# Kernel tuning notes

Measured on AMD Instinct MI355X. Metric: run time of the kernel, lower is better.

The kernel has to match this reference:

```python
import jax, jax.numpy as jnp
import numpy as np

N_HEADS = 16
ROPE_BASE = 10000.0


def apply_rope(x):
    # x: [B, H, T, D]; rotate interleaved pairs along last dim, positions along T
    B, H, T, D = x.shape
    half = D // 2
    inv_freq = 1.0 / (ROPE_BASE ** (jnp.arange(0, half, dtype=jnp.float32) * 2.0 / D))
    angles = jnp.arange(T, dtype=jnp.float32)[:, None] * inv_freq[None, :]  # [T, half]
    cos = jnp.cos(angles).astype(x.dtype)  # [T, half]
    sin = jnp.sin(angles).astype(x.dtype)
    xp = x.reshape(B, H, T, half, 2)
    x1, x2 = xp[..., 0], xp[..., 1]
    out = jnp.stack([x1 * cos - x2 * sin, x1 * sin + x2 * cos], axis=-1)
    return out.reshape(B, H, T, D)


def setup_inputs() -> dict:
    key = jax.random.key(0)
    k1, k2, k3 = jax.random.split(key, 3)
    C = 1024
    x = jax.random.normal(k1, (2, 2048, C), dtype=jnp.float32)
    w_qkv = jax.random.normal(k2, (C, 3 * C), dtype=jnp.float32) * (1.0 / np.sqrt(C))
    w_out = jax.random.normal(k3, (C, C), dtype=jnp.float32) * (1.0 / np.sqrt(C))
    return {"x": x, "w_qkv": w_qkv, "w_out": w_out}


def reference(x, w_qkv, w_out):
    B, T, C = x.shape
    H = N_HEADS
    D = C // H
    qkv = (x @ w_qkv).reshape(B, T, 3, H, D)
    q, k, v = qkv[:, :, 0], qkv[:, :, 1], qkv[:, :, 2]  # [B, T, H, D]
    q = jnp.transpose(q, (0, 2, 1, 3))  # [B, H, T, D]
    k = jnp.transpose(k, (0, 2, 1, 3))
    v = jnp.transpose(v, (0, 2, 1, 3))
    q = apply_rope(q)
    k = apply_rope(k)
    scale = 1.0 / np.sqrt(D)
    scores = jnp.einsum('bhqd,bhkd->bhqk', q, k) * scale
    causal = jnp.tril(jnp.ones((T, T), dtype=bool))
    scores = jnp.where(causal, scores, jnp.finfo(scores.dtype).min)
    attn = jax.nn.softmax(scores, axis=-1)
    out = jnp.einsum('bhqk,bhkd->bhqd', attn, v)  # [B, H, T, D]
    out = jnp.transpose(out, (0, 2, 1, 3)).reshape(B, T, C)
    return out @ w_out
```

## Files before the change

### kernel.cpp

```cpp
#include <hip/hip_runtime.h>
#include <hip/hip_bf16.h>

typedef __attribute__((ext_vector_type(8))) short v8s;
typedef __attribute__((ext_vector_type(4))) float v4f;
typedef __attribute__((ext_vector_type(16))) float v16f;

typedef const __attribute__((address_space(1))) void* gas_ptr;
typedef __attribute__((address_space(3))) void* las_ptr;

#define MFMA16(a, b, c) __builtin_amdgcn_mfma_f32_16x16x32_bf16((a), (b), (c), 0, 0, 0)
#define MFMA32(a, b, c) __builtin_amdgcn_mfma_f32_32x32x16_bf16((a), (b), (c), 0, 0, 0)

__device__ __forceinline__ void gload_lds16(const void* g, void* l) {
  __builtin_amdgcn_global_load_lds((gas_ptr)g, (las_ptr)l, 16, 0, 0);
}

__device__ __forceinline__ unsigned short f2bf(float f) {
  unsigned int u = __float_as_uint(f);
  u += 0x7FFFu + ((u >> 16) & 1u);
  return (unsigned short)(u >> 16);
}
__device__ __forceinline__ float bf2f(unsigned short h) {
  return __uint_as_float(((unsigned int)h) << 16);
}

__device__ __forceinline__ unsigned cvt_pk_bf16(float lo, float hi) {
  unsigned r;
  asm("v_cvt_pk_bf16_f32 %0, %1, %2" : "=v"(r) : "v"(lo), "v"(hi));
  return r;
}

__global__ __launch_bounds__(256) void k_convert(const float* __restrict__ in,
                                                 unsigned short* __restrict__ out, int n4) {
  int i = blockIdx.x * 256 + threadIdx.x;
  if (i >= n4) return;
  float4 v = ((const float4*)in)[i];
  ushort4 o;
  o.x = f2bf(v.x); o.y = f2bf(v.y); o.z = f2bf(v.z); o.w = f2bf(v.w);
  ((ushort4*)out)[i] = o;
}

__global__ __launch_bounds__(256) void k_transpose_convert(const float* __restrict__ in,
                                                           unsigned short* __restrict__ out,
                                                           int R, int C) {
  __shared__ __attribute__((aligned(16))) unsigned short tb[64 * 72];
  const int r0 = blockIdx.y * 64, c0 = blockIdx.x * 64;
  const int tid = threadIdx.x;
#pragma unroll
  for (int j = 0; j < 4; ++j) {
    int slot = tid + 256 * j;
    int row = slot >> 4, q4 = (slot & 15) * 4;
    float4 v = *(const float4*)&in[(size_t)(r0 + row) * C + c0 + q4];
    ushort4 o;
    o.x = f2bf(v.x); o.y = f2bf(v.y); o.z = f2bf(v.z); o.w = f2bf(v.w);
    *(ushort4*)&tb[row * 72 + q4] = o;
  }
  __syncthreads();
#pragma unroll
  for (int j = 0; j < 4; ++j) {
    int slot = tid + 256 * j;
    int crow = slot >> 4, t4 = (slot & 15) * 4;
    ushort4 o;
    o.x = tb[(t4 + 0) * 72 + crow];
    o.y = tb[(t4 + 1) * 72 + crow];
    o.z = tb[(t4 + 2) * 72 + crow];
    o.w = tb[(t4 + 3) * 72 + crow];
    *(ushort4*)&out[(size_t)(c0 + crow) * R + r0 + t4] = o;
  }
}

template <bool F32OUT, int BN, int WAVES_M, int WAVES_N>
__global__ __launch_bounds__(256) void k_gemm(const unsigned short* __restrict__ A,
                                              const unsigned short* __restrict__ Bt,
                                              void* __restrict__ Cout,
                                              int M, int N, int K) {
  constexpr int WM = 128 / (WAVES_M * 16);
  constexpr int WN = BN / (WAVES_N * 16);
  __shared__ __attribute__((aligned(16))) unsigned short As[128 * 32];
  __shared__ __attribute__((aligned(16))) unsigned short Bs[BN * 32];
  const int tid = threadIdx.x;
  const int w = tid >> 6, l = tid & 63, g = l >> 4, c = l & 15;
  const int wr = w / WAVES_N, wc = w % WAVES_N;

  const int nwg = gridDim.x * gridDim.y;
  const int orig = blockIdx.y * gridDim.x + blockIdx.x;
  const int wgid = (orig & 7) * (nwg >> 3) + (orig >> 3);
  const int mt = (wgid / gridDim.x) * 128;
  const int nt = (wgid % gridDim.x) * BN;

  const int rowc = l >> 2, kslot = (l & 3) * 8;

  v4f acc[WM][WN];
#pragma unroll
  for (int m = 0; m < WM; ++m)
#pragma unroll
    for (int n = 0; n < WN; ++n) acc[m][n] = (v4f){0.f, 0.f, 0.f, 0.f};

  constexpr int NCHUNK = 8 + BN / 16;
  for (int kt = 0; kt < K; kt += 32) {
    __syncthreads();
#pragma unroll
    for (int ch = 0; ch < NCHUNK; ch += 4) {
      int cc = ch + w;
      if (cc < 8)
        gload_lds16(&A[(size_t)(mt + cc * 16 + rowc) * K + kt + kslot], &As[cc * 512]);
      else
        gload_lds16(&Bt[(size_t)(nt + (cc - 8) * 16 + rowc) * K + kt + kslot],
                    &Bs[(cc - 8) * 512]);
    }
    __syncthreads();
    v8s af[WM], bfr[WN];
#pragma unroll
    for (int m = 0; m < WM; ++m)
      af[m] = *(const v8s*)&As[(wr * (WM * 16) + m * 16 + c) * 32 + g * 8];
#pragma unroll
    for (int n = 0; n < WN; ++n)
      bfr[n] = *(const v8s*)&Bs[(wc * (WN * 16) + n * 16 + c) * 32 + g * 8];
#pragma unroll
    for (int m = 0; m < WM; ++m)
#pragma unroll
      for (int n = 0; n < WN; ++n)
        acc[m][n] = MFMA16(af[m], bfr[n], acc[m][n]);
  }

#pragma unroll
  for (int m = 0; m < WM; ++m)
#pragma unroll
    for (int n = 0; n < WN; ++n)
#pragma unroll
      for (int r = 0; r < 4; ++r) {
        int row = mt + wr * (WM * 16) + m * 16 + g * 4 + r;
        int col = nt + wc * (WN * 16) + n * 16 + c;
        if (F32OUT)
          ((float*)Cout)[(size_t)row * N + col] = acc[m][n][r];
        else
          ((unsigned short*)Cout)[(size_t)row * N + col] = f2bf(acc[m][n][r]);
      }
}

__global__ __launch_bounds__(256) void k_post(const unsigned short* __restrict__ qkv,
                                              unsigned short* __restrict__ qp,
                                              unsigned short* __restrict__ kp,
                                              unsigned short* __restrict__ vp) {
  __shared__ float2 cs[64 * 32];
  __shared__ __attribute__((aligned(16))) unsigned short vt[64 * 72];
  const int bh = blockIdx.y;
  const int b = bh >> 4, hd = bh & 15;
  const int t0 = blockIdx.x * 64;
  const int tid = threadIdx.x;

#pragma unroll
  for (int e = 0; e < 8; ++e) {
    int idx = tid + 256 * e;
    int tl = idx >> 5, i = idx & 31;
    float invf = exp2f(-(float)i * 0.41524101186092034f);
    float ang = (float)(t0 + tl) * invf;
    float s, cc;
    sincosf(ang, &s, &cc);
    cs[idx] = make_float2(cc, s);
  }
#pragma unroll
  for (int j = 0; j < 2; ++j) {
    int slot = tid + 256 * j;
    int row = slot >> 3, c8 = (slot & 7) * 8;
    v8s vv = *(const v8s*)&qkv[(size_t)(b * 2048 + t0 + row) * 3072 + 2048 + hd * 64 + c8];
    *(v8s*)&vt[row * 72 + c8] = vv;
  }
  __syncthreads();

#pragma unroll
  for (int j = 0; j < 2; ++j) {
    int slot = tid + 256 * j;
    int row = slot >> 3, d0 = (slot & 7) * 8;
    int t = t0 + row;
    size_t base = (size_t)(b * 2048 + t) * 3072 + hd * 64;
    const int tile = t >> 5, c32 = t & 31, kd = d0 >> 4, hh = (d0 >> 3) & 1;
    const size_t pidx = (size_t)bh * 131072 + (tile * 4 + kd) * 512 + (hh * 32 + c32) * 8;
#pragma unroll
    for (int which = 0; which < 2; ++which) {
      const float qsc = which ? 1.0f : 0.18033688011112042f;
      v8s vq = *(const v8s*)&qkv[base + which * 1024 + d0];
      union { unsigned short s[8]; v8s v; } uo;
#pragma unroll
      for (int p = 0; p < 4; ++p) {
        float2 sc = cs[row * 32 + d0 / 2 + p];
        float x1 = bf2f((unsigned short)vq[2 * p]);
        float x2 = bf2f((unsigned short)vq[2 * p + 1]);
        uo.s[2 * p]     = f2bf((x1 * sc.x - x2 * sc.y) * qsc);
        uo.s[2 * p + 1] = f2bf((x1 * sc.y + x2 * sc.x) * qsc);
      }
      unsigned short* dst = which ? kp : qp;
      *(v8s*)&dst[pidx] = uo.v;
    }
  }

#pragma unroll
  for (int jj = 0; jj < 2; ++jj) {
    int idx = tid + 256 * jj;
    int tl = idx >> 8, kc = (idx >> 7) & 1, md = (idx >> 6) & 1;
    int lp = idx & 63, hh = lp >> 5, c32 = lp & 31;
    int d = md * 32 + c32;
    int brow = tl * 32 + kc * 16 + hh * 4;
    union { unsigned short s[8]; v8s v; } uo;
#pragma unroll
    for (int jh = 0; jh < 2; ++jh)
#pragma unroll
      for (int e = 0; e < 4; ++e)
        uo.s[jh * 4 + e] = vt[(brow + jh * 8 + e) * 72 + d];
    int tileG = (t0 >> 5) + tl;
    *(v8s*)&vp[(size_t)bh * 131072 + ((tileG * 2 + kc) * 2 + md) * 512 + lp * 8] = uo.v;
  }
}

__global__ __launch_bounds__(64) void k_attn(const unsigned short* __restrict__ qp,
                                             const unsigned short* __restrict__ kp,
                                             const unsigned short* __restrict__ vp,
                                             unsigned short* __restrict__ ao,
                                             char* __restrict__ part) {
  const int bid = (int)blockIdx.x;
  const int xcd = bid & 7, s2 = bid >> 3;
  const int bh = xcd + 8 * (s2 / 160);
  const int idx = 159 - (s2 % 160);
  int j, s;
  if (idx >= 96)      { j = 48 + ((idx - 96) >> 2); s = (idx - 96) & 3; }
  else if (idx >= 48) { j = 32 + (idx - 48) / 3;    s = (idx - 48) % 3; }
  else if (idx >= 16) { j = 16 + ((idx - 16) >> 1); s = (idx - 16) & 1; }
  else                { j = idx;                    s = 0; }
  const int t0 = s * 16;
  const int t1 = (t0 + 16 < j + 1) ? (t0 + 16) : (j + 1);

  const int l = threadIdx.x;
  const int c32 = l & 31, hh = l >> 5;
  const unsigned short* Qb = qp + (size_t)bh * 131072 + j * 4 * 512;
  const unsigned short* Kb = kp + (size_t)bh * 131072;
  const unsigned short* Vb = vp + (size_t)bh * 131072;

  v8s bq[4];
#pragma unroll
  for (int kd = 0; kd < 4; ++kd) bq[kd] = *(const v8s*)&Qb[kd * 512 + l * 8];

  v16f ot0 = {0,0,0,0,0,0,0,0,0,0,0,0,0,0,0,0};
  v16f ot1 = {0,0,0,0,0,0,0,0,0,0,0,0,0,0,0,0};
  float m2 = -1e30f, lsl = 0.f;

  v8s ak[4], av0[2][2], av1[2][2];
#pragma unroll
  for (int kd = 0; kd < 4; ++kd) ak[kd] = *(const v8s*)&Kb[(t0 * 4 + kd) * 512 + l * 8];
#pragma unroll
  for (int kc = 0; kc < 2; ++kc)
#pragma unroll
    for (int md = 0; md < 2; ++md)
      av0[kc][md] = *(const v8s*)&Vb[((t0 * 2 + kc) * 2 + md) * 512 + l * 8];

  auto TILE = [&](int t, v8s (&avc)[2][2], v8s (&avn)[2][2]) {
    v16f st = {0,0,0,0,0,0,0,0,0,0,0,0,0,0,0,0};
    __builtin_amdgcn_s_setprio(1);
#pragma unroll
    for (int kd = 0; kd < 4; ++kd) st = MFMA32(ak[kd], bq[kd], st);
    __builtin_amdgcn_s_setprio(0);

    if (t + 1 < t1) {
#pragma unroll
      for (int kd = 0; kd < 4; ++kd)
        ak[kd] = *(const v8s*)&Kb[((t + 1) * 4 + kd) * 512 + l * 8];
#pragma unroll
      for (int kc = 0; kc < 2; ++kc)
#pragma unroll
        for (int md = 0; md < 2; ++md)
          avn[kc][md] = *(const v8s*)&Vb[(((t + 1) * 2 + kc) * 2 + md) * 512 + l * 8];
    }

    if (t == j) {
#pragma unroll
      for (int r = 0; r < 16; ++r) {
        int rloc = (r & 3) + 8 * (r >> 2) + 4 * hh;
        st[r] = (rloc <= c32) ? st[r] : -1e30f;
      }
    }

    float a0 = fmaxf(st[0], st[1]),   a1 = fmaxf(st[2], st[3]);
    float a2 = fmaxf(st[4], st[5]),   a3 = fmaxf(st[6], st[7]);
    float a4 = fmaxf(st[8], st[9]),   a5 = fmaxf(st[10], st[11]);
    float a6 = fmaxf(st[12], st[13]), a7 = fmaxf(st[14], st[15]);
    float b0m = fmaxf(fmaxf(a0, a1), fmaxf(a2, a3));
    float b1m = fmaxf(fmaxf(a4, a5), fmaxf(a6, a7));
    float pm = fmaxf(b0m, b1m);
    if (!__all(pm <= m2 + 8.f)) {
      float pmw = fmaxf(pm, __shfl_xor(pm, 32));
      float mn = fmaxf(m2, pmw);
      float al = exp2f(m2 - mn);
      m2 = mn;
      lsl *= al;
      ot0 *= al;
      ot1 *= al;
    }

#pragma unroll
    for (int r = 0; r < 16; ++r) st[r] = exp2f(st[r] - m2);
    float e0 = st[0] + st[1],   e1 = st[2] + st[3];
    float e2 = st[4] + st[5],   e3 = st[6] + st[7];
    float e4 = st[8] + st[9],   e5 = st[10] + st[11];
    float e6 = st[12] + st[13], e7 = st[14] + st[15];
    float f0 = e0 + e1, f1 = e2 + e3, f2 = e4 + e5, f3 = e6 + e7;
    lsl += (f0 + f1) + (f2 + f3);

    unsigned wd[8];
#pragma unroll
    for (int i = 0; i < 8; ++i) wd[i] = cvt_pk_bf16(st[2 * i], st[2 * i + 1]);
    union { unsigned u[4]; v8s v; } pb0, pb1;
    pb0.u[0] = wd[0]; pb0.u[1] = wd[1]; pb0.u[2] = wd[2]; pb0.u[3] = wd[3];
    pb1.u[0] = wd[4]; pb1.u[1] = wd[5]; pb1.u[2] = wd[6]; pb1.u[3] = wd[7];

    __builtin_amdgcn_s_setprio(1);
    ot0 = MFMA32(avc[0][0], pb0.v, ot0);
    ot1 = MFMA32(avc[0][1], pb0.v, ot1);
    ot0 = MFMA32(avc[1][0], pb1.v, ot0);
    ot1 = MFMA32(avc[1][1], pb1.v, ot1);
    __builtin_amdgcn_s_setprio(0);
  };

  int t = t0;
  for (; t + 1 < t1; t += 2) {
    TILE(t,     av0, av1);
    TILE(t + 1, av1, av0);
  }
  if (t < t1) TILE(t, av0, av1);

  const float ls = lsl + __shfl_xor(lsl, 32);
  const float inv = 1.f / ls;
  if (j < 16) {
    const int b = bh >> 4, hd = bh & 15;
    const int tq = j * 32 + c32;
    unsigned short* aop = ao + (size_t)(b * 2048 + tq) * 1024 + hd * 64;
#pragma unroll
    for (int md = 0; md < 2; ++md)
#pragma unroll
      for (int q = 0; q < 4; ++q) {
        const v16f& o = md ? ot1 : ot0;
        unsigned w0 = cvt_pk_bf16(o[4 * q + 0] * inv, o[4 * q + 1] * inv);
        unsigned w1 = cvt_pk_bf16(o[4 * q + 2] * inv, o[4 * q + 3] * inv);
        int d = md * 32 + 8 * q + 4 * hh;
        *(uint2*)&aop[d] = make_uint2(w0, w1);
      }
  } else {
    char* slot = part + ((size_t)bh * 160 + idx) * 4352;
#pragma unroll
    for (int md = 0; md < 2; ++md)
#pragma unroll
      for (int i = 0; i < 8; ++i) {
        const v16f& o = md ? ot1 : ot0;
        union { _Float16 h[2]; unsigned u; } pk;
        pk.h[0] = (_Float16)(o[2 * i] * inv);
        pk.h[1] = (_Float16)(o[2 * i + 1] * inv);
        *(unsigned*)(slot + ((md * 8 + i) * 64 + l) * 4) = pk.u;
      }
    if (hh == 0) {
      *(float*)(slot + 4096 + c32 * 4) = m2;
      *(float*)(slot + 4224 + c32 * 4) = ls;
    }
  }
}

__global__ __launch_bounds__(64) void k_comb(const char* __restrict__ part,
                                             unsigned short* __restrict__ ao) {
  const int bh = blockIdx.y;
  const int j = 16 + (int)blockIdx.x;
  const int g = j >> 4;
  const int nch = g + 1;
  const int l = threadIdx.x, c32 = l & 31, hh = l >> 5;
  const int baseg = (g == 1) ? 16 : (g == 2) ? 48 : 96;
  const int ord0 = baseg + (j - 16 * g) * nch;
  const char* base = part + (size_t)bh * 160 * 4352;

  float ms[4], lsv[4], wsc[4];
  float mfin = -1e30f;
#pragma unroll
  for (int s = 0; s < 4; ++s) {
    if (s < nch) {
      const char* sl = base + (size_t)(ord0 + s) * 4352;
      ms[s] = *(const float*)(sl + 4096 + c32 * 4);
      lsv[s] = *(const float*)(sl + 4224 + c32 * 4);
      mfin = fmaxf(mfin, ms[s]);
    }
  }
  float lfin = 0.f;
#pragma unroll
  for (int s = 0; s < 4; ++s) {
    if (s < nch) {
      wsc[s] = lsv[s] * exp2f(ms[s] - mfin);
      lfin += wsc[s];
    }
  }
  const float inv = 1.f / lfin;
#pragma unroll
  for (int s = 0; s < 4; ++s)
    if (s < nch) wsc[s] *= inv;

  const int b = bh >> 4, hd = bh & 15;
  const int t = j * 32 + c32;
  unsigned short* aop = ao + (size_t)(b * 2048 + t) * 1024 + hd * 64;
#pragma unroll
  for (int md = 0; md < 2; ++md)
#pragma unroll
    for (int q4 = 0; q4 < 4; ++q4) {
      const int w0 = md * 8 + 2 * q4;
      float a0 = 0.f, a1 = 0.f, a2 = 0.f, a3 = 0.f;
#pragma unroll
      for (int s = 0; s < 4; ++s) {
        if (s < nch) {
          const char* sl = base + (size_t)(ord0 + s) * 4352;
          unsigned u0 = *(const unsigned*)(sl + ((w0 + 0) * 64 + l) * 4);
          unsigned u1 = *(const unsigned*)(sl + ((w0 + 1) * 64 + l) * 4);
          union { unsigned u; _Float16 h[2]; } p0, p1;
          p0.u = u0; p1.u = u1;
          a0 += (float)p0.h[0] * wsc[s];
          a1 += (float)p0.h[1] * wsc[s];
          a2 += (float)p1.h[0] * wsc[s];
          a3 += (float)p1.h[1] * wsc[s];
        }
      }
      unsigned o0 = cvt_pk_bf16(a0, a1);
      unsigned o1 = cvt_pk_bf16(a2, a3);
      int d = md * 32 + 8 * q4 + 4 * hh;
      *(uint2*)&aop[d] = make_uint2(o0, o1);
    }
}

extern "C" void kernel_launch(void* const* d_in, const int* in_sizes, int n_in,
                              void* d_out, int out_size, void* d_ws, size_t ws_size,
                              hipStream_t stream) {
  const float* x     = (const float*)d_in[0];
  const float* w_qkv = (const float*)d_in[1];
  const float* w_out = (const float*)d_in[2];
  float* out = (float*)d_out;

  char* ws = (char*)d_ws;
  unsigned short* xbf = (unsigned short*)(ws);
  unsigned short* wqT = (unsigned short*)(ws + 8388608);
  unsigned short* woT = (unsigned short*)(ws + 14680064);
  unsigned short* qkv = (unsigned short*)(ws + 16777216);
  unsigned short* qp  = (unsigned short*)(ws + 41943040);
  unsigned short* kp  = (unsigned short*)(ws + 50331648);
  unsigned short* vp  = (unsigned short*)(ws + 58720256);
  char* part = (char*)(ws + 16777216);

  k_convert<<<4096, 256, 0, stream>>>(x, xbf, 1048576);
  k_transpose_convert<<<dim3(48, 16), 256, 0, stream>>>(w_qkv, wqT, 1024, 3072);
  k_transpose_convert<<<dim3(16, 16), 256, 0, stream>>>(w_out, woT, 1024, 1024);
  k_gemm<false, 128, 2, 2><<<dim3(24, 32), 256, 0, stream>>>(xbf, wqT, qkv, 4096, 3072, 1024);
  k_post<<<dim3(32, 32), 256, 0, stream>>>(qkv, qp, kp, vp);
  k_attn<<<5120, 64, 0, stream>>>(qp, kp, vp, xbf , part);
  k_comb<<<dim3(48, 32), 64, 0, stream>>>(part, xbf);
  k_gemm<true, 64, 4, 1><<<dim3(16, 32), 256, 0, stream>>>(xbf, woT, (void*)out, 4096, 1024, 1024);
}
```

Baseline: 139.5 us.

## Process two KV tiles per iteration with a merged online-softmax update

Restructures the attention inner loop so each iteration computes scores for two 32-key tiles at once. The two tiles share one max check and rescale, and their QK and PV MFMAs are interleaved. K and V for the next pair are prefetched, with V loads moved after the PV MFMAs. This is meant to raise MFMA issue density and halve the per-tile softmax bookkeeping, at the cost of more live registers, which could lower occupancy.

```diff
diff --git a/kernel.cpp b/kernel.cpp
--- a/kernel.cpp
+++ b/kernel.cpp
@@ -243,48 +243,66 @@
   v16f ot1 = {0,0,0,0,0,0,0,0,0,0,0,0,0,0,0,0};
   float m2 = -1e30f, lsl = 0.f;
 
-  v8s ak[4], av0[2][2], av1[2][2];
-#pragma unroll
-  for (int kd = 0; kd < 4; ++kd) ak[kd] = *(const v8s*)&Kb[(t0 * 4 + kd) * 512 + l * 8];
+  v8s ak[2][4], av[2][2][2];
+#pragma unroll
+  for (int kd = 0; kd < 4; ++kd) ak[0][kd] = *(const v8s*)&Kb[((size_t)t0 * 4 + kd) * 512 + l * 8];
 #pragma unroll
   for (int kc = 0; kc < 2; ++kc)
 #pragma unroll
     for (int md = 0; md < 2; ++md)
-      av0[kc][md] = *(const v8s*)&Vb[((t0 * 2 + kc) * 2 + md) * 512 + l * 8];
-
-  auto TILE = [&](int t, v8s (&avc)[2][2], v8s (&avn)[2][2]) {
-    v16f st = {0,0,0,0,0,0,0,0,0,0,0,0,0,0,0,0};
+      av[0][kc][md] = *(const v8s*)&Vb[(((size_t)t0 * 2 + kc) * 2 + md) * 512 + l * 8];
+  if (t0 + 1 < t1) {
+#pragma unroll
+    for (int kd = 0; kd < 4; ++kd)
+      ak[1][kd] = *(const v8s*)&Kb[((size_t)(t0 + 1) * 4 + kd) * 512 + l * 8];
+#pragma unroll
+    for (int kc = 0; kc < 2; ++kc)
+#pragma unroll
+      for (int md = 0; md < 2; ++md)
+        av[1][kc][md] = *(const v8s*)&Vb[(((size_t)(t0 + 1) * 2 + kc) * 2 + md) * 512 + l * 8];
+  }
+
+  int t = t0;
+  for (; t + 1 < t1; t += 2) {
+    v16f st0 = {0,0,0,0,0,0,0,0,0,0,0,0,0,0,0,0};
+    v16f st1 = {0,0,0,0,0,0,0,0,0,0,0,0,0,0,0,0};
     __builtin_amdgcn_s_setprio(1);
 #pragma unroll
-    for (int kd = 0; kd < 4; ++kd) st = MFMA32(ak[kd], bq[kd], st);
+    for (int kd = 0; kd < 4; ++kd) {
+      st0 = MFMA32(ak[0][kd], bq[kd], st0);
+      st1 = MFMA32(ak[1][kd], bq[kd], st1);
+    }
     __builtin_amdgcn_s_setprio(0);
 
-    if (t + 1 < t1) {
+    if (t + 2 < t1) {
 #pragma unroll
       for (int kd = 0; kd < 4; ++kd)
-        ak[kd] = *(const v8s*)&Kb[((t + 1) * 4 + kd) * 512 + l * 8];
-#pragma unroll
-      for (int kc = 0; kc < 2; ++kc)
-#pragma unroll
-        for (int md = 0; md < 2; ++md)
-          avn[kc][md] = *(const v8s*)&Vb[(((t + 1) * 2 + kc) * 2 + md) * 512 + l * 8];
-    }
-
-    if (t == j) {
+        ak[0][kd] = *(const v8s*)&Kb[((size_t)(t + 2) * 4 + kd) * 512 + l * 8];
+    }
+    if (t + 3 < t1) {
+#pragma unroll
+      for (int kd = 0; kd < 4; ++kd)
+        ak[1][kd] = *(const v8s*)&Kb[((size_t)(t + 3) * 4 + kd) * 512 + l * 8];
+    }
+
+    if (t + 1 == j) {
 #pragma unroll
       for (int r = 0; r < 16; ++r) {
         int rloc = (r & 3) + 8 * (r >> 2) + 4 * hh;
-        st[r] = (rloc <= c32) ? st[r] : -1e30f;
-      }
-    }
-
-    float a0 = fmaxf(st[0], st[1]),   a1 = fmaxf(st[2], st[3]);
-    float a2 = fmaxf(st[4], st[5]),   a3 = fmaxf(st[6], st[7]);
-    float a4 = fmaxf(st[8], st[9]),   a5 = fmaxf(st[10], st[11]);
-    float a6 = fmaxf(st[12], st[13]), a7 = fmaxf(st[14], st[15]);
-    float b0m = fmaxf(fmaxf(a0, a1), fmaxf(a2, a3));
-    float b1m = fmaxf(fmaxf(a4, a5), fmaxf(a6, a7));
-    float pm = fmaxf(b0m, b1m);
+        st1[r] = (rloc <= c32) ? st1[r] : -1e30f;
+      }
+    }
+
+    float a0 = fmaxf(fmaxf(st0[0], st0[1]), fmaxf(st0[2], st0[3]));
+    float a1 = fmaxf(fmaxf(st0[4], st0[5]), fmaxf(st0[6], st0[7]));
+    float a2 = fmaxf(fmaxf(st0[8], st0[9]), fmaxf(st0[10], st0[11]));
+    float a3 = fmaxf(fmaxf(st0[12], st0[13]), fmaxf(st0[14], st0[15]));
+    float b0 = fmaxf(fmaxf(st1[0], st1[1]), fmaxf(st1[2], st1[3]));
+    float b1 = fmaxf(fmaxf(st1[4], st1[5]), fmaxf(st1[6], st1[7]));
+    float b2 = fmaxf(fmaxf(st1[8], st1[9]), fmaxf(st1[10], st1[11]));
+    float b3 = fmaxf(fmaxf(st1[12], st1[13]), fmaxf(st1[14], st1[15]));
+    float pm = fmaxf(fmaxf(fmaxf(a0, a1), fmaxf(a2, a3)),
+                     fmaxf(fmaxf(b0, b1), fmaxf(b2, b3)));
     if (!__all(pm <= m2 + 8.f)) {
       float pmw = fmaxf(pm, __shfl_xor(pm, 32));
       float mn = fmaxf(m2, pmw);
@@ -296,13 +314,95 @@
     }
 
 #pragma unroll
+    for (int r = 0; r < 16; ++r) st0[r] = exp2f(st0[r] - m2);
+#pragma unroll
+    for (int r = 0; r < 16; ++r) st1[r] = exp2f(st1[r] - m2);
+    {
+      float e0 = (st0[0] + st0[1]) + (st0[2] + st0[3]);
+      float e1 = (st0[4] + st0[5]) + (st0[6] + st0[7]);
+      float e2 = (st0[8] + st0[9]) + (st0[10] + st0[11]);
+      float e3 = (st0[12] + st0[13]) + (st0[14] + st0[15]);
+      float f0 = (st1[0] + st1[1]) + (st1[2] + st1[3]);
+      float f1 = (st1[4] + st1[5]) + (st1[6] + st1[7]);
+      float f2 = (st1[8] + st1[9]) + (st1[10] + st1[11]);
+      float f3 = (st1[12] + st1[13]) + (st1[14] + st1[15]);
+      lsl += ((e0 + e1) + (e2 + e3)) + ((f0 + f1) + (f2 + f3));
+    }
+
+    unsigned wd0[8], wd1[8];
+#pragma unroll
+    for (int i = 0; i < 8; ++i) wd0[i] = cvt_pk_bf16(st0[2 * i], st0[2 * i + 1]);
+#pragma unroll
+    for (int i = 0; i < 8; ++i) wd1[i] = cvt_pk_bf16(st1[2 * i], st1[2 * i + 1]);
+    union { unsigned u[4]; v8s v; } p00, p01, p10, p11;
+    p00.u[0] = wd0[0]; p00.u[1] = wd0[1]; p00.u[2] = wd0[2]; p00.u[3] = wd0[3];
+    p01.u[0] = wd0[4]; p01.u[1] = wd0[5]; p01.u[2] = wd0[6]; p01.u[3] = wd0[7];
+    p10.u[0] = wd1[0]; p10.u[1] = wd1[1]; p10.u[2] = wd1[2]; p10.u[3] = wd1[3];
+    p11.u[0] = wd1[4]; p11.u[1] = wd1[5]; p11.u[2] = wd1[6]; p11.u[3] = wd1[7];
+
+    __builtin_amdgcn_s_setprio(1);
+    ot0 = MFMA32(av[0][0][0], p00.v, ot0);
+    ot1 = MFMA32(av[0][0][1], p00.v, ot1);
+    ot0 = MFMA32(av[0][1][0], p01.v, ot0);
+    ot1 = MFMA32(av[0][1][1], p01.v, ot1);
+    ot0 = MFMA32(av[1][0][0], p10.v, ot0);
+    ot1 = MFMA32(av[1][0][1], p10.v, ot1);
+    ot0 = MFMA32(av[1][1][0], p11.v, ot0);
+    ot1 = MFMA32(av[1][1][1], p11.v, ot1);
+    __builtin_amdgcn_s_setprio(0);
+
+    if (t + 2 < t1) {
+#pragma unroll
+      for (int kc = 0; kc < 2; ++kc)
+#pragma unroll
+        for (int md = 0; md < 2; ++md)
+          av[0][kc][md] = *(const v8s*)&Vb[(((size_t)(t + 2) * 2 + kc) * 2 + md) * 512 + l * 8];
+    }
+    if (t + 3 < t1) {
+#pragma unroll
+      for (int kc = 0; kc < 2; ++kc)
+#pragma unroll
+        for (int md = 0; md < 2; ++md)
+          av[1][kc][md] = *(const v8s*)&Vb[(((size_t)(t + 3) * 2 + kc) * 2 + md) * 512 + l * 8];
+    }
+  }
+
+  if (t < t1) {
+    v16f st = {0,0,0,0,0,0,0,0,0,0,0,0,0,0,0,0};
+    __builtin_amdgcn_s_setprio(1);
+#pragma unroll
+    for (int kd = 0; kd < 4; ++kd) st = MFMA32(ak[0][kd], bq[kd], st);
+    __builtin_amdgcn_s_setprio(0);
+
+    if (t == j) {
+#pragma unroll
+      for (int r = 0; r < 16; ++r) {
+        int rloc = (r & 3) + 8 * (r >> 2) + 4 * hh;
+        st[r] = (rloc <= c32) ? st[r] : -1e30f;
+      }
+    }
+
+    float a0 = fmaxf(fmaxf(st[0], st[1]), fmaxf(st[2], st[3]));
+    float a1 = fmaxf(fmaxf(st[4], st[5]), fmaxf(st[6], st[7]));
+    float a2 = fmaxf(fmaxf(st[8], st[9]), fmaxf(st[10], st[11]));
+    float a3 = fmaxf(fmaxf(st[12], st[13]), fmaxf(st[14], st[15]));
+    float pm = fmaxf(fmaxf(a0, a1), fmaxf(a2, a3));
+    if (!__all(pm <= m2 + 8.f)) {
+      float pmw = fmaxf(pm, __shfl_xor(pm, 32));
+      float mn = fmaxf(m2, pmw);
+      float al = exp2f(m2 - mn);
+      m2 = mn;
+      lsl *= al;
+      ot0 *= al;
+      ot1 *= al;
+    }
+#pragma unroll
     for (int r = 0; r < 16; ++r) st[r] = exp2f(st[r] - m2);
-    float e0 = st[0] + st[1],   e1 = st[2] + st[3];
-    float e2 = st[4] + st[5],   e3 = st[6] + st[7];
-    float e4 = st[8] + st[9],   e5 = st[10] + st[11];
-    float e6 = st[12] + st[13], e7 = st[14] + st[15];
-    float f0 = e0 + e1, f1 = e2 + e3, f2 = e4 + e5, f3 = e6 + e7;
-    lsl += (f0 + f1) + (f2 + f3);
+    float e0 = (st[0] + st[1]) + (st[2] + st[3]);
+    float e1 = (st[4] + st[5]) + (st[6] + st[7]);
+    float e2 = (st[8] + st[9]) + (st[10] + st[11]);
+    float e3 = (st[12] + st[13]) + (st[14] + st[15]);
+    lsl += (e0 + e1) + (e2 + e3);
 
     unsigned wd[8];
 #pragma unroll
@@ -312,19 +412,12 @@
     pb1.u[0] = wd[4]; pb1.u[1] = wd[5]; pb1.u[2] = wd[6]; pb1.u[3] = wd[7];
 
     __builtin_amdgcn_s_setprio(1);
-    ot0 = MFMA32(avc[0][0], pb0.v, ot0);
-    ot1 = MFMA32(avc[0][1], pb0.v, ot1);
-    ot0 = MFMA32(avc[1][0], pb1.v, ot0);
-    ot1 = MFMA32(avc[1][1], pb1.v, ot1);
+    ot0 = MFMA32(av[0][0][0], pb0.v, ot0);
+    ot1 = MFMA32(av[0][0][1], pb0.v, ot1);
+    ot0 = MFMA32(av[0][1][0], pb1.v, ot0);
+    ot1 = MFMA32(av[0][1][1], pb1.v, ot1);
     __builtin_amdgcn_s_setprio(0);
-  };
-
-  int t = t0;
-  for (; t + 1 < t1; t += 2) {
-    TILE(t,     av0, av1);
-    TILE(t + 1, av1, av0);
-  }
-  if (t < t1) TILE(t, av0, av1);
+  }
 
   const float ls = lsl + __shfl_xor(lsl, 32);
   const float inv = 1.f / ls;
```

After: 139.6 us, median of 4. About the same (+0.1%).
